# Kernel optimization log

Measured on AMD Instinct MI355X. Metric: run time of the kernel, lower is better.

Reference implementation:

```python
import jax, jax.numpy as jnp
import numpy as np

N = 100000   # nodes
E = 640000   # edges
D = 128      # hidden/in channels
G = 64       # graphs in batch
L = 3        # GCN layers (n_layers - 1)
EPS = 1e-5   # batchnorm eps


def _bn(h, gamma, beta):
    # BatchNorm1d in train mode: biased variance over the node axis
    m = h.mean(axis=0)
    v = h.var(axis=0)
    return (h - m) * jax.lax.rsqrt(v + EPS) * gamma + beta


def setup_inputs() -> dict:
    key = jax.random.key(0)
    ks = jax.random.split(key, 20)
    s = 1.0 / np.sqrt(D)
    inp = {
        "x": jax.random.normal(ks[0], (N, D), jnp.float32),
        "edge_index": jax.random.randint(ks[1], (2, E), 0, N, dtype=jnp.int64),
        "batch": jnp.sort(jax.random.randint(ks[2], (N,), 0, G, dtype=jnp.int64)),
        # encoder MLP (2 layers, batchnorm+relu between)
        "enc_W1": jax.random.normal(ks[3], (D, D), jnp.float32) * s,
        "enc_b1": jnp.zeros((D,), jnp.float32),
        "enc_g": jnp.ones((D,), jnp.float32),
        "enc_be": jnp.zeros((D,), jnp.float32),
        "enc_W2": jax.random.normal(ks[4], (D, D), jnp.float32) * s,
        "enc_b2": jnp.zeros((D,), jnp.float32),
        # stacked GCN layer params
        "conv_W": jax.random.normal(ks[5], (L, D, D), jnp.float32) * s,
        "conv_b": jnp.zeros((L, D), jnp.float32),
        "bn_g": jnp.ones((L, D), jnp.float32),
        "bn_b": jnp.zeros((L, D), jnp.float32),
        # MLPReadout: 128 -> 64 -> 32 -> 1
        "ro_W1": jax.random.normal(ks[6], (D, D // 2), jnp.float32) * s,
        "ro_b1": jnp.zeros((D // 2,), jnp.float32),
        "ro_W2": jax.random.normal(ks[7], (D // 2, D // 4), jnp.float32) * (1.0 / np.sqrt(D // 2)),
        "ro_b2": jnp.zeros((D // 4,), jnp.float32),
        "ro_W3": jax.random.normal(ks[8], (D // 4, 1), jnp.float32) * (1.0 / np.sqrt(D // 4)),
        "ro_b3": jnp.zeros((1,), jnp.float32),
    }
    return inp


def reference(x, edge_index, batch, enc_W1, enc_b1, enc_g, enc_be, enc_W2, enc_b2,
              conv_W, conv_b, bn_g, bn_b, ro_W1, ro_b1, ro_W2, ro_b2, ro_W3, ro_b3):
    src, dst = edge_index[0], edge_index[1]

    # gcn_norm (add_self_loops=False): deg from target column, sym normalization
    deg = jax.ops.segment_sum(jnp.ones((E,), x.dtype), dst, num_segments=N)
    dinv = jnp.where(deg > 0, jax.lax.rsqrt(jnp.maximum(deg, 1.0)), 0.0)
    norm = (dinv[src] * dinv[dst])[:, None]  # [E,1]

    # encoder MLP: Linear -> BN -> ReLU -> Linear
    h = jax.nn.relu(_bn(x @ enc_W1 + enc_b1, enc_g, enc_be))
    h = h @ enc_W2 + enc_b2

    # stacked GCN layers with BN + ReLU + residual
    for l in range(L):
        hw = h @ conv_W[l]                         # [N,D]
        agg = jax.ops.segment_sum(hw[src] * norm, dst, num_segments=N)
        agg = agg + conv_b[l]
        h = h + jax.nn.relu(_bn(agg, bn_g[l], bn_b[l]))

    # scatter-sum pooling per graph
    hg = jax.ops.segment_sum(h, batch, num_segments=G)  # [G,D]

    # MLP readout
    y = jax.nn.relu(hg @ ro_W1 + ro_b1)
    y = jax.nn.relu(y @ ro_W2 + ro_b2)
    y = y @ ro_W3 + ro_b3
    return y
```

## Files before the change

### kernel.cpp

```cpp
#include <hip/hip_runtime.h>
#include <hip/hip_bf16.h>

#define NN 100000
#define NE 640000
#define DD 128
#define NG 64
#define NL 3
#define BN_EPS 1e-5f

typedef unsigned short u16;
typedef unsigned int u32;
typedef __attribute__((ext_vector_type(8))) short short8;
typedef __attribute__((ext_vector_type(4))) float f32x4;

__device__ __forceinline__ void atomAddG(float* p, float v) { unsafeAtomicAdd(p, v); }

__device__ __forceinline__ float bf_lo(u32 u) { return __uint_as_float(u << 16); }
__device__ __forceinline__ float bf_hi(u32 u) { return __uint_as_float(u & 0xffff0000u); }
__device__ __forceinline__ float bfs(short s) { return __uint_as_float(((u32)(u16)s) << 16); }
__device__ __forceinline__ u16 bfb(float f) {
    __hip_bfloat16 b = __float2bfloat16(f);
    return *(u16*)&b;
}
__device__ __forceinline__ u32 pk(float a, float b) {
    return (u32)bfb(a) | ((u32)bfb(b) << 16);
}

__global__ void k_degI(const int* __restrict__ dst, int* __restrict__ degI) {
    int e = blockIdx.x * 256 + threadIdx.x;
    if (e < NE) atomicAdd(&degI[dst[e]], 1);
}

__global__ void k_dinv(const int* __restrict__ degI, float* __restrict__ dinv) {
    int i = blockIdx.x * 256 + threadIdx.x;
    if (i < NN) { int d = degI[i]; dinv[i] = d > 0 ? rsqrtf((float)d) : 0.f; }
}

__global__ void k_scan1(const int* __restrict__ degI, int* __restrict__ offs, int* __restrict__ bsum) {
    __shared__ int ls[256];
    int t = threadIdx.x;
    int i = blockIdx.x * 256 + t;
    int v = (i < NN) ? degI[i] : 0;
    ls[t] = v;
    __syncthreads();
    for (int off = 1; off < 256; off <<= 1) {
        int u = (t >= off) ? ls[t - off] : 0;
        __syncthreads();
        ls[t] += u;
        __syncthreads();
    }
    if (i < NN) offs[i] = ls[t] - v;
    if (t == 255) bsum[blockIdx.x] = ls[255];
}

__global__ void k_scan2(int* __restrict__ bsum, int nb) {
    __shared__ int ls[512];
    int t = threadIdx.x;
    int v = (t < nb) ? bsum[t] : 0;
    ls[t] = v;
    __syncthreads();
    for (int off = 1; off < 512; off <<= 1) {
        int u = (t >= off) ? ls[t - off] : 0;
        __syncthreads();
        ls[t] += u;
        __syncthreads();
    }
    if (t < nb) bsum[t] = ls[t] - v;
}

__global__ void k_scan3(int* __restrict__ offs, const int* __restrict__ bsum) {
    int i = blockIdx.x * 256 + threadIdx.x;
    if (i < NN) offs[i] += bsum[blockIdx.x];
    if (i == 0) offs[NN] = NE;
}

__global__ void k_place(const int* __restrict__ src, const int* __restrict__ dst,
                        const int* __restrict__ offs, int* __restrict__ cur,
                        u32* __restrict__ eIdx) {
    int e = blockIdx.x * 256 + threadIdx.x;
    if (e < NE) {
        int d = dst[e];
        int pos = offs[d] + atomicAdd(&cur[d], 1);
        eIdx[pos] = (u32)src[e];
    }
}

__global__ void k_prepW(const float* __restrict__ W1, const float* __restrict__ W2,
                        const float* __restrict__ CW, u16* __restrict__ wtb) {
    int m = blockIdx.x >> 3;
    const float* src = (m == 0) ? W1 : (m == 1) ? W2 : CW + (size_t)(m - 2) * 16384;
    u16* dst = wtb + (size_t)m * 16384;
    int base = (blockIdx.x & 7) * 2048 + threadIdx.x;
#pragma unroll
    for (int i = 0; i < 8; ++i) {
        int idx = base + i * 256;
        int k = idx >> 7, n = idx & 127;
        dst[n * 128 + k] = bfb(src[idx]);
    }
}

template <int MODE>
__global__ __launch_bounds__(256) void k_mm(
    const void* __restrict__ Av, const u16* __restrict__ Wt,
    const float* __restrict__ bias, const float* __restrict__ scl, const float* __restrict__ shf,
    const float* __restrict__ dinv,
    u16* __restrict__ Cb, float* __restrict__ Cf,
    float* __restrict__ sSum, float* __restrict__ sSq)
{
    __shared__ float lC[64 * 128];
    int tid = threadIdx.x;
    int l = tid & 63, w = tid >> 6;
    int lr = l & 15, lg = l >> 4;
    int wcol = (w & 1) * 64, wrow = (w >> 1) * 32;

    short8 Bf[4][4];
#pragma unroll
    for (int ct = 0; ct < 4; ++ct)
#pragma unroll
        for (int ks = 0; ks < 4; ++ks)
            Bf[ct][ks] = *(const short8*)(Wt + (size_t)(wcol + ct * 16 + lr) * 128 + ks * 32 + lg * 8);

    f32x4 acc[2][4];
#pragma unroll
    for (int rg = 0; rg < 2; ++rg)
#pragma unroll
        for (int ct = 0; ct < 4; ++ct)
            acc[rg][ct] = (f32x4){0.f, 0.f, 0.f, 0.f};

    int rbase = blockIdx.x * 64 + wrow;
#pragma unroll
    for (int rg = 0; rg < 2; ++rg) {
        int row = rbase + rg * 16 + lr;
        row = min(row, NN - 1);
        short8 Af[4];
        if (MODE == 1) {
            const float* af = (const float*)Av + (size_t)row * 128 + lg * 8;
#pragma unroll
            for (int ks = 0; ks < 4; ++ks) {
                float4 v0 = *(const float4*)(af + ks * 32);
                float4 v1 = *(const float4*)(af + ks * 32 + 4);
                short8 o;
                o[0] = (short)bfb(v0.x); o[1] = (short)bfb(v0.y);
                o[2] = (short)bfb(v0.z); o[3] = (short)bfb(v0.w);
                o[4] = (short)bfb(v1.x); o[5] = (short)bfb(v1.y);
                o[6] = (short)bfb(v1.z); o[7] = (short)bfb(v1.w);
                Af[ks] = o;
            }
        } else {
            const u16* ap = (const u16*)Av + (size_t)row * 128 + lg * 8;
#pragma unroll
            for (int ks = 0; ks < 4; ++ks) Af[ks] = *(const short8*)(ap + ks * 32);
            if (MODE == 2) {
#pragma unroll
                for (int ks = 0; ks < 4; ++ks) {
                    int cb = ks * 32 + lg * 8;
                    float4 s0 = *(const float4*)(scl + cb), s1 = *(const float4*)(scl + cb + 4);
                    float4 f0 = *(const float4*)(shf + cb), f1 = *(const float4*)(shf + cb + 4);
                    short8 a = Af[ks], o;
                    o[0] = (short)bfb(fmaxf(0.f, bfs(a[0]) * s0.x + f0.x));
                    o[1] = (short)bfb(fmaxf(0.f, bfs(a[1]) * s0.y + f0.y));
                    o[2] = (short)bfb(fmaxf(0.f, bfs(a[2]) * s0.z + f0.z));
                    o[3] = (short)bfb(fmaxf(0.f, bfs(a[3]) * s0.w + f0.w));
                    o[4] = (short)bfb(fmaxf(0.f, bfs(a[4]) * s1.x + f1.x));
                    o[5] = (short)bfb(fmaxf(0.f, bfs(a[5]) * s1.y + f1.y));
                    o[6] = (short)bfb(fmaxf(0.f, bfs(a[6]) * s1.z + f1.z));
                    o[7] = (short)bfb(fmaxf(0.f, bfs(a[7]) * s1.w + f1.w));
                    Af[ks] = o;
                }
            }
        }
#pragma unroll
        for (int ks = 0; ks < 4; ++ks)
#pragma unroll
            for (int ct = 0; ct < 4; ++ct)
                acc[rg][ct] = __builtin_amdgcn_mfma_f32_16x16x32_bf16(Af[ks], Bf[ct][ks], acc[rg][ct], 0, 0, 0);
    }

    if (MODE == 2) {
#pragma unroll
        for (int ct = 0; ct < 4; ++ct) {
            float bc = bias[wcol + ct * 16 + lr];
#pragma unroll
            for (int rg = 0; rg < 2; ++rg)
#pragma unroll
                for (int j = 0; j < 4; ++j) acc[rg][ct][j] += bc;
        }
    }

#pragma unroll
    for (int rg = 0; rg < 2; ++rg)
#pragma unroll
        for (int ct = 0; ct < 4; ++ct)
#pragma unroll
            for (int j = 0; j < 4; ++j)
                lC[(wrow + rg * 16 + lg * 4 + j) * 128 + wcol + ct * 16 + lr] = acc[rg][ct][j];
    __syncthreads();

    float cs[4] = {0.f, 0.f, 0.f, 0.f}, cq[4] = {0.f, 0.f, 0.f, 0.f};
#pragma unroll
    for (int i = 0; i < 8; ++i) {
        int eidx = i * 1024 + tid * 4;
        int lrow = eidx >> 7;
        int col = eidx & 127;
        int grow = blockIdx.x * 64 + lrow;
        if (grow < NN) {
            float4 v = *(float4*)(lC + eidx);
            if (MODE == 0) {
                float dd = dinv[grow];
                v.x *= dd; v.y *= dd; v.z *= dd; v.w *= dd;
                u32* Cs = (u32*)Cb;
                *(uint2*)(Cs + (size_t)grow * 64 + (col >> 1)) =
                    make_uint2(pk(v.x, v.y), pk(v.z, v.w));
            } else {
                uint2 o = make_uint2(pk(v.x, v.y), pk(v.z, v.w));
                *(uint2*)(Cb + (size_t)grow * 128 + col) = o;
                if (MODE == 2) *(float4*)(Cf + (size_t)grow * 128 + col) = v;
                if (MODE == 1) {
                    cs[0] += v.x; cs[1] += v.y; cs[2] += v.z; cs[3] += v.w;
                    cq[0] += v.x * v.x; cq[1] += v.y * v.y; cq[2] += v.z * v.z; cq[3] += v.w * v.w;
                }
            }
        }
    }

    if (MODE == 1) {
        __syncthreads();
        int g = tid >> 5, c0 = (tid & 31) * 4;
#pragma unroll
        for (int cc = 0; cc < 4; ++cc) {
            lC[g * 128 + c0 + cc] = cs[cc];
            lC[1024 + g * 128 + c0 + cc] = cq[cc];
        }
        __syncthreads();
        if (tid < 128) {
            float s = 0.f, q = 0.f;
#pragma unroll
            for (int g2 = 0; g2 < 8; ++g2) { s += lC[g2 * 128 + tid]; q += lC[1024 + g2 * 128 + tid]; }
            atomAddG(&sSum[tid], s);
            atomAddG(&sSq[tid], q);
        }
    }
}

__global__ void k_bnfinal(const float* __restrict__ sSum, const float* __restrict__ sSq,
                          const float* __restrict__ g, const float* __restrict__ be,
                          float* __restrict__ scl, float* __restrict__ shf) {
    int c = threadIdx.x;
    float m = sSum[c] * (1.0f / NN);
    float v = sSq[c] * (1.0f / NN) - m * m;
    float s = g[c] * rsqrtf(v + BN_EPS);
    scl[c] = s;
    shf[c] = be[c] - m * s;
}

__global__ __launch_bounds__(256) void k_agg(
    const u32* __restrict__ hwb,
    const u32* __restrict__ eIdx, const int* __restrict__ offs,
    const float* __restrict__ dinv,
    u32* __restrict__ aggb, float* __restrict__ sSum, float* __restrict__ sSq)
{
    int tid = threadIdx.x;
    int lane = tid & 63;
    int wav = tid >> 6;
    int gw = blockIdx.x * 4 + wav;
    int nw = gridDim.x * 4;
    float sx0 = 0.f, sx1 = 0.f, sq0 = 0.f, sq1 = 0.f;

    for (int d0 = gw * 4; d0 < NN; d0 += nw * 4) {
        int o0 = offs[d0], o1 = offs[d0 + 1], o2 = offs[d0 + 2], o3 = offs[d0 + 3], o4 = offs[d0 + 4];
        int st[4] = {o0, o1, o2, o3};
        int len[4] = {o1 - o0, o2 - o1, o3 - o2, o4 - o3};
        int mcl[4];
#pragma unroll
        for (int d = 0; d < 4; ++d) mcl[d] = max(len[d] - 1, 0);
        int mx = max(max(len[0], len[1]), max(len[2], len[3]));
        float ax[4] = {0.f, 0.f, 0.f, 0.f}, ay[4] = {0.f, 0.f, 0.f, 0.f};
        for (int jb = 0; jb < mx; jb += 8) {
            u32 ii[4][8];
#pragma unroll
            for (int d = 0; d < 4; ++d)
#pragma unroll
                for (int q = 0; q < 8; ++q)
                    ii[d][q] = eIdx[min(st[d] + min(jb + q, mcl[d]), NE - 1)];
            u32 uu[4][8];
#pragma unroll
            for (int d = 0; d < 4; ++d)
#pragma unroll
                for (int q = 0; q < 8; ++q)
                    uu[d][q] = hwb[(size_t)ii[d][q] * 64 + lane];
#pragma unroll
            for (int d = 0; d < 4; ++d)
#pragma unroll
                for (int q = 0; q < 8; ++q) {
                    bool v = (jb + q) < len[d];
                    ax[d] += v ? bf_lo(uu[d][q]) : 0.f;
                    ay[d] += v ? bf_hi(uu[d][q]) : 0.f;
                }
        }
#pragma unroll
        for (int d = 0; d < 4; ++d) {
            float dd = dinv[d0 + d];
            float vx = ax[d] * dd, vy = ay[d] * dd;
            aggb[(size_t)(d0 + d) * 64 + lane] = pk(vx, vy);
            sx0 += vx; sx1 += vy;
            sq0 += vx * vx; sq1 += vy * vy;
        }
    }

    __shared__ float ls[512], lq[512];
    ls[wav * 128 + lane * 2] = sx0;
    ls[wav * 128 + lane * 2 + 1] = sx1;
    lq[wav * 128 + lane * 2] = sq0;
    lq[wav * 128 + lane * 2 + 1] = sq1;
    __syncthreads();
    if (tid < 128) {
        float s = ls[tid] + ls[tid + 128] + ls[tid + 256] + ls[tid + 384];
        float q = lq[tid] + lq[tid + 128] + lq[tid + 256] + lq[tid + 384];
        atomAddG(&sSum[tid], s);
        atomAddG(&sSq[tid], q);
    }
}

__global__ __launch_bounds__(256) void k_update(
    float* __restrict__ h, const u32* __restrict__ aggb,
    const float* __restrict__ scl, const float* __restrict__ shf,
    u32* __restrict__ hb)
{
    int i = blockIdx.x * 256 + threadIdx.x;
    int c0 = (i * 4) & 127;
    uint2 a = *(const uint2*)(aggb + (size_t)i * 2);
    float4 hv = *(float4*)(h + (size_t)i * 4);
    float4 sv = *(const float4*)(scl + c0);
    float4 fv = *(const float4*)(shf + c0);
    hv.x += fmaxf(0.f, bf_lo(a.x) * sv.x + fv.x);
    hv.y += fmaxf(0.f, bf_hi(a.x) * sv.y + fv.y);
    hv.z += fmaxf(0.f, bf_lo(a.y) * sv.z + fv.z);
    hv.w += fmaxf(0.f, bf_hi(a.y) * sv.w + fv.w);
    *(float4*)(h + (size_t)i * 4) = hv;
    *(uint2*)(hb + (size_t)i * 2) = make_uint2(pk(hv.x, hv.y), pk(hv.z, hv.w));
}

__global__ __launch_bounds__(256) void k_pool(
    const float* __restrict__ h, const u32* __restrict__ aggb,
    const float* __restrict__ scl, const float* __restrict__ shf,
    const int* __restrict__ batch, float* __restrict__ hg)
{
    __shared__ float lsum[128];
    int tid = threadIdx.x;
    int c = tid & 127, half = tid >> 7;
    float sc = scl[c], sf = shf[c];
    int r0 = blockIdx.x * 64;
    int rend = min(r0 + 64, NN);
    int b0 = batch[r0], b1 = batch[rend - 1];

    if (b0 == b1) {
        float acc = 0.f;
        for (int r = r0 + half; r < rend; r += 2) {
            u32 a = aggb[(size_t)r * 64 + (c >> 1)];
            float av = (c & 1) ? bf_hi(a) : bf_lo(a);
            acc += h[(size_t)r * 128 + c] + fmaxf(0.f, av * sc + sf);
        }
        if (half) lsum[c] = acc;
        __syncthreads();
        if (!half) atomAddG(&hg[b0 * DD + c], acc + lsum[c]);
    } else {
        float acc = 0.f;
        int cur = batch[r0 + half];
        for (int r = r0 + half; r < rend; r += 2) {
            int b = batch[r];
            if (b != cur) { atomAddG(&hg[cur * DD + c], acc); acc = 0.f; cur = b; }
            u32 a = aggb[(size_t)r * 64 + (c >> 1)];
            float av = (c & 1) ? bf_hi(a) : bf_lo(a);
            acc += h[(size_t)r * 128 + c] + fmaxf(0.f, av * sc + sf);
        }
        atomAddG(&hg[cur * DD + c], acc);
    }
}

__global__ __launch_bounds__(128) void k_readout(
    const float* __restrict__ hg,
    const float* __restrict__ W1, const float* __restrict__ b1,
    const float* __restrict__ W2, const float* __restrict__ b2,
    const float* __restrict__ W3, const float* __restrict__ b3,
    float* __restrict__ out) {
    __shared__ float a0[128], a1[64], a2[32];
    int g = blockIdx.x, t = threadIdx.x;
    a0[t] = hg[g * DD + t];
    __syncthreads();
    if (t < 64) {
        float s = b1[t];
        for (int k = 0; k < 128; ++k) s += a0[k] * W1[k * 64 + t];
        a1[t] = fmaxf(s, 0.f);
    }
    __syncthreads();
    if (t < 32) {
        float s = b2[t];
        for (int k = 0; k < 64; ++k) s += a1[k] * W2[k * 32 + t];
        a2[t] = fmaxf(s, 0.f);
    }
    __syncthreads();
    if (t == 0) {
        float s = b3[0];
        for (int k = 0; k < 32; ++k) s += a2[k] * W3[k];
        out[g] = s;
    }
}

extern "C" void kernel_launch(void* const* d_in, const int* in_sizes, int n_in,
                              void* d_out, int out_size, void* d_ws, size_t ws_size,
                              hipStream_t stream) {
    const float* x      = (const float*)d_in[0];
    const int*   ei     = (const int*)d_in[1];
    const int*   batch  = (const int*)d_in[2];
    const float* enc_W1 = (const float*)d_in[3];
    const float* enc_g  = (const float*)d_in[5];
    const float* enc_be = (const float*)d_in[6];
    const float* enc_W2 = (const float*)d_in[7];
    const float* enc_b2 = (const float*)d_in[8];
    const float* conv_W = (const float*)d_in[9];
    const float* bn_g   = (const float*)d_in[11];
    const float* bn_b   = (const float*)d_in[12];
    const float* ro_W1  = (const float*)d_in[13];
    const float* ro_b1  = (const float*)d_in[14];
    const float* ro_W2  = (const float*)d_in[15];
    const float* ro_b2  = (const float*)d_in[16];
    const float* ro_W3  = (const float*)d_in[17];
    const float* ro_b3  = (const float*)d_in[18];

    const int* srcI = ei;
    const int* dstI = ei + NE;

    float* ws   = (float*)d_ws;
    float* h    = ws;
    u32*   aggb = (u32*)(ws + 12800000);
    u32*   hb   = (u32*)(ws + 19200000);
    u32*   t1b  = (u32*)(ws + 25600000);
    u16*   wtb  = (u16*)(ws + 32000000);
    float* dinv = ws + 32050000;
    float* sSum = ws + 32150000;
    float* sSq  = sSum + 128;
    float* scl  = sSum + 256;
    float* shf  = sSum + 384;
    float* hg   = ws + 32150512;
    int*   offs = (int*)(ws + 32160000);
    int*   degI = (int*)(ws + 32270000);
    int*   bsum = (int*)(ws + 32370000);
    u32*   eIdx = (u32*)(ws + 32380000);

    u16* tb16 = (u16*)aggb;

    k_prepW<<<40, 256, 0, stream>>>(enc_W1, enc_W2, conv_W, wtb);

    hipMemsetAsync(degI, 0, NN * sizeof(int), stream);
    k_degI<<<2500, 256, 0, stream>>>(dstI, degI);
    k_dinv<<<391, 256, 0, stream>>>(degI, dinv);
    k_scan1<<<391, 256, 0, stream>>>(degI, offs, bsum);
    k_scan2<<<1, 512, 0, stream>>>(bsum, 391);
    k_scan3<<<391, 256, 0, stream>>>(offs, bsum);
    hipMemsetAsync(degI, 0, NN * sizeof(int), stream);
    k_place<<<2500, 256, 0, stream>>>(srcI, dstI, offs, degI, eIdx);

    hipMemsetAsync(sSum, 0, 256 * sizeof(float), stream);
    k_mm<1><<<1563, 256, 0, stream>>>(x, wtb, nullptr, nullptr, nullptr, nullptr, tb16, nullptr, sSum, sSq);
    k_bnfinal<<<1, 128, 0, stream>>>(sSum, sSq, enc_g, enc_be, scl, shf);
    k_mm<2><<<1563, 256, 0, stream>>>(tb16, wtb + 16384, enc_b2, scl, shf, nullptr, (u16*)hb, h, nullptr, nullptr);

    for (int l = 0; l < NL; ++l) {
        k_mm<0><<<1563, 256, 0, stream>>>((const u16*)hb, wtb + (size_t)(2 + l) * 16384,
                                          nullptr, nullptr, nullptr, dinv, (u16*)t1b, nullptr, nullptr, nullptr);
        hipMemsetAsync(sSum, 0, 256 * sizeof(float), stream);
        k_agg<<<2048, 256, 0, stream>>>(t1b, eIdx, offs, dinv, aggb, sSum, sSq);
        k_bnfinal<<<1, 128, 0, stream>>>(sSum, sSq, bn_g + l * DD, bn_b + l * DD, scl, shf);
        if (l < NL - 1)
            k_update<<<12500, 256, 0, stream>>>(h, aggb, scl, shf, hb);
    }

    hipMemsetAsync(hg, 0, NG * DD * sizeof(float), stream);
    k_pool<<<1563, 256, 0, stream>>>(h, aggb, scl, shf, batch, hg);
    k_readout<<<NG, 128, 0, stream>>>(hg, ro_W1, ro_b1, ro_W2, ro_b2, ro_W3, ro_b3, (float*)d_out);
}
```

Baseline: 543.4 us.

## Drop fp32 residual stream and keep hidden state only in bf16

The fp32 copy of the hidden state h is removed. The residual update, the encoder output and pooling now read and write only the bf16 buffer, which cuts per-layer memory traffic in k_update and k_pool and removes the fp32 store in the second encoder matmul. The dinv kernel is folded into the first scan kernel, and the BN stat accumulators are zeroed inside k_bnfinal instead of by a separate memset per layer. The cost is that residual accumulation now happens in bf16, which adds rounding error across layers.

Result: slower. 584.0 us (+7.5%).

```diff
diff --git a/kernel.cpp b/kernel.cpp
--- a/kernel.cpp
+++ b/kernel.cpp
@@ -31,16 +31,13 @@
     if (e < NE) atomicAdd(&degI[dst[e]], 1);
 }
 
-__global__ void k_dinv(const int* __restrict__ degI, float* __restrict__ dinv) {
-    int i = blockIdx.x * 256 + threadIdx.x;
-    if (i < NN) { int d = degI[i]; dinv[i] = d > 0 ? rsqrtf((float)d) : 0.f; }
-}
-
-__global__ void k_scan1(const int* __restrict__ degI, int* __restrict__ offs, int* __restrict__ bsum) {
+__global__ void k_scan1(const int* __restrict__ degI, int* __restrict__ offs, int* __restrict__ bsum,
+                        float* __restrict__ dinv) {
     __shared__ int ls[256];
     int t = threadIdx.x;
     int i = blockIdx.x * 256 + t;
     int v = (i < NN) ? degI[i] : 0;
+    if (i < NN) dinv[i] = v > 0 ? rsqrtf((float)v) : 0.f;
     ls[t] = v;
     __syncthreads();
     for (int off = 1; off < 256; off <<= 1) {
@@ -104,7 +101,7 @@
     const void* __restrict__ Av, const u16* __restrict__ Wt,
     const float* __restrict__ bias, const float* __restrict__ scl, const float* __restrict__ shf,
     const float* __restrict__ dinv,
-    u16* __restrict__ Cb, float* __restrict__ Cf,
+    u16* __restrict__ Cb,
     float* __restrict__ sSum, float* __restrict__ sSq)
 {
     __shared__ float lC[64 * 128];
@@ -212,9 +209,8 @@
                 *(uint2*)(Cs + (size_t)grow * 64 + (col >> 1)) =
                     make_uint2(pk(v.x, v.y), pk(v.z, v.w));
             } else {
-                uint2 o = make_uint2(pk(v.x, v.y), pk(v.z, v.w));
-                *(uint2*)(Cb + (size_t)grow * 128 + col) = o;
-                if (MODE == 2) *(float4*)(Cf + (size_t)grow * 128 + col) = v;
+                *(uint2*)(Cb + (size_t)grow * 128 + col) =
+                    make_uint2(pk(v.x, v.y), pk(v.z, v.w));
                 if (MODE == 1) {
                     cs[0] += v.x; cs[1] += v.y; cs[2] += v.z; cs[3] += v.w;
                     cq[0] += v.x * v.x; cq[1] += v.y * v.y; cq[2] += v.z * v.z; cq[3] += v.w * v.w;
@@ -242,7 +238,7 @@
     }
 }
 
-__global__ void k_bnfinal(const float* __restrict__ sSum, const float* __restrict__ sSq,
+__global__ void k_bnfinal(float* __restrict__ sSum, float* __restrict__ sSq,
                           const float* __restrict__ g, const float* __restrict__ be,
                           float* __restrict__ scl, float* __restrict__ shf) {
     int c = threadIdx.x;
@@ -251,6 +247,8 @@
     float s = g[c] * rsqrtf(v + BN_EPS);
     scl[c] = s;
     shf[c] = be[c] - m * s;
+    sSum[c] = 0.f;
+    sSq[c] = 0.f;
 }
 
 __global__ __launch_bounds__(256) void k_agg(
@@ -322,26 +320,24 @@
 }
 
 __global__ __launch_bounds__(256) void k_update(
-    float* __restrict__ h, const u32* __restrict__ aggb,
-    const float* __restrict__ scl, const float* __restrict__ shf,
-    u32* __restrict__ hb)
+    u32* __restrict__ hb, const u32* __restrict__ aggb,
+    const float* __restrict__ scl, const float* __restrict__ shf)
 {
     int i = blockIdx.x * 256 + threadIdx.x;
     int c0 = (i * 4) & 127;
     uint2 a = *(const uint2*)(aggb + (size_t)i * 2);
-    float4 hv = *(float4*)(h + (size_t)i * 4);
+    uint2 hv = *(const uint2*)(hb + (size_t)i * 2);
     float4 sv = *(const float4*)(scl + c0);
     float4 fv = *(const float4*)(shf + c0);
-    hv.x += fmaxf(0.f, bf_lo(a.x) * sv.x + fv.x);
-    hv.y += fmaxf(0.f, bf_hi(a.x) * sv.y + fv.y);
-    hv.z += fmaxf(0.f, bf_lo(a.y) * sv.z + fv.z);
-    hv.w += fmaxf(0.f, bf_hi(a.y) * sv.w + fv.w);
-    *(float4*)(h + (size_t)i * 4) = hv;
-    *(uint2*)(hb + (size_t)i * 2) = make_uint2(pk(hv.x, hv.y), pk(hv.z, hv.w));
+    float x = bf_lo(hv.x) + fmaxf(0.f, bf_lo(a.x) * sv.x + fv.x);
+    float y = bf_hi(hv.x) + fmaxf(0.f, bf_hi(a.x) * sv.y + fv.y);
+    float z = bf_lo(hv.y) + fmaxf(0.f, bf_lo(a.y) * sv.z + fv.z);
+    float u = bf_hi(hv.y) + fmaxf(0.f, bf_hi(a.y) * sv.w + fv.w);
+    *(uint2*)(hb + (size_t)i * 2) = make_uint2(pk(x, y), pk(z, u));
 }
 
 __global__ __launch_bounds__(256) void k_pool(
-    const float* __restrict__ h, const u32* __restrict__ aggb,
+    const u32* __restrict__ hb, const u32* __restrict__ aggb,
     const float* __restrict__ scl, const float* __restrict__ shf,
     const int* __restrict__ batch, float* __restrict__ hg)
 {
@@ -357,8 +353,10 @@
         float acc = 0.f;
         for (int r = r0 + half; r < rend; r += 2) {
             u32 a = aggb[(size_t)r * 64 + (c >> 1)];
+            u32 hv = hb[(size_t)r * 64 + (c >> 1)];
             float av = (c & 1) ? bf_hi(a) : bf_lo(a);
-            acc += h[(size_t)r * 128 + c] + fmaxf(0.f, av * sc + sf);
+            float hvv = (c & 1) ? bf_hi(hv) : bf_lo(hv);
+            acc += hvv + fmaxf(0.f, av * sc + sf);
         }
         if (half) lsum[c] = acc;
         __syncthreads();
@@ -370,8 +368,10 @@
             int b = batch[r];
             if (b != cur) { atomAddG(&hg[cur * DD + c], acc); acc = 0.f; cur = b; }
             u32 a = aggb[(size_t)r * 64 + (c >> 1)];
+            u32 hv = hb[(size_t)r * 64 + (c >> 1)];
             float av = (c & 1) ? bf_hi(a) : bf_lo(a);
-            acc += h[(size_t)r * 128 + c] + fmaxf(0.f, av * sc + sf);
+            float hvv = (c & 1) ? bf_hi(hv) : bf_lo(hv);
+            acc += hvv + fmaxf(0.f, av * sc + sf);
         }
         atomAddG(&hg[cur * DD + c], acc);
     }
@@ -431,21 +431,20 @@
     const int* dstI = ei + NE;
 
     float* ws   = (float*)d_ws;
-    float* h    = ws;
-    u32*   aggb = (u32*)(ws + 12800000);
-    u32*   hb   = (u32*)(ws + 19200000);
-    u32*   t1b  = (u32*)(ws + 25600000);
-    u16*   wtb  = (u16*)(ws + 32000000);
-    float* dinv = ws + 32050000;
-    float* sSum = ws + 32150000;
+    u32*   aggb = (u32*)ws;
+    u32*   hb   = (u32*)(ws + 6400000);
+    u32*   t1b  = (u32*)(ws + 12800000);
+    u16*   wtb  = (u16*)(ws + 19200000);
+    float* dinv = ws + 19250000;
+    float* sSum = ws + 19351000;
     float* sSq  = sSum + 128;
     float* scl  = sSum + 256;
     float* shf  = sSum + 384;
-    float* hg   = ws + 32150512;
-    int*   offs = (int*)(ws + 32160000);
-    int*   degI = (int*)(ws + 32270000);
-    int*   bsum = (int*)(ws + 32370000);
-    u32*   eIdx = (u32*)(ws + 32380000);
+    float* hg   = ws + 19352000;
+    int*   offs = (int*)(ws + 19361000);
+    int*   degI = (int*)(ws + 19462000);
+    int*   bsum = (int*)(ws + 19563000);
+    u32*   eIdx = (u32*)(ws + 19564000);
 
     u16* tb16 = (u16*)aggb;
 
@@ -453,29 +452,27 @@
 
     hipMemsetAsync(degI, 0, NN * sizeof(int), stream);
     k_degI<<<2500, 256, 0, stream>>>(dstI, degI);
-    k_dinv<<<391, 256, 0, stream>>>(degI, dinv);
-    k_scan1<<<391, 256, 0, stream>>>(degI, offs, bsum);
+    k_scan1<<<391, 256, 0, stream>>>(degI, offs, bsum, dinv);
     k_scan2<<<1, 512, 0, stream>>>(bsum, 391);
     k_scan3<<<391, 256, 0, stream>>>(offs, bsum);
     hipMemsetAsync(degI, 0, NN * sizeof(int), stream);
     k_place<<<2500, 256, 0, stream>>>(srcI, dstI, offs, degI, eIdx);
 
     hipMemsetAsync(sSum, 0, 256 * sizeof(float), stream);
-    k_mm<1><<<1563, 256, 0, stream>>>(x, wtb, nullptr, nullptr, nullptr, nullptr, tb16, nullptr, sSum, sSq);
+    k_mm<1><<<1563, 256, 0, stream>>>(x, wtb, nullptr, nullptr, nullptr, nullptr, tb16, sSum, sSq);
     k_bnfinal<<<1, 128, 0, stream>>>(sSum, sSq, enc_g, enc_be, scl, shf);
-    k_mm<2><<<1563, 256, 0, stream>>>(tb16, wtb + 16384, enc_b2, scl, shf, nullptr, (u16*)hb, h, nullptr, nullptr);
+    k_mm<2><<<1563, 256, 0, stream>>>(tb16, wtb + 16384, enc_b2, scl, shf, nullptr, (u16*)hb, nullptr, nullptr);
 
     for (int l = 0; l < NL; ++l) {
         k_mm<0><<<1563, 256, 0, stream>>>((const u16*)hb, wtb + (size_t)(2 + l) * 16384,
-                                          nullptr, nullptr, nullptr, dinv, (u16*)t1b, nullptr, nullptr, nullptr);
-        hipMemsetAsync(sSum, 0, 256 * sizeof(float), stream);
+                                          nullptr, nullptr, nullptr, dinv, (u16*)t1b, nullptr, nullptr);
         k_agg<<<2048, 256, 0, stream>>>(t1b, eIdx, offs, dinv, aggb, sSum, sSq);
         k_bnfinal<<<1, 128, 0, stream>>>(sSum, sSq, bn_g + l * DD, bn_b + l * DD, scl, shf);
         if (l < NL - 1)
-            k_update<<<12500, 256, 0, stream>>>(h, aggb, scl, shf, hb);
+            k_update<<<12500, 256, 0, stream>>>(hb, aggb, scl, shf);
     }
 
     hipMemsetAsync(hg, 0, NG * DD * sizeof(float), stream);
-    k_pool<<<1563, 256, 0, stream>>>(h, aggb, scl, shf, batch, hg);
+    k_pool<<<1563, 256, 0, stream>>>(hb, aggb, scl, shf, batch, hg);
     k_readout<<<NG, 128, 0, stream>>>(hg, ro_W1, ro_b1, ro_W2, ro_b2, ro_W3, ro_b3, (float*)d_out);
 }
```
